# Performance work log

Measured on AMD Instinct MI355X. Metric: run time of the kernel, lower is better.

## Reference

```python
import jax, jax.numpy as jnp
import numpy as np

B, T, E, H = 4, 2048, 1024, 16
HD = E // H  # 64


def setup_inputs() -> dict:
    key = jax.random.key(0)
    ks = jax.random.split(key, 7)
    s = 0.02
    return {
        "values": jax.random.normal(ks[0], (B, T, E), jnp.float32),
        "keys": jax.random.normal(ks[1], (B, T, E), jnp.float32),
        "query": jax.random.normal(ks[2], (B, T, E), jnp.float32),
        "Wv": jax.random.normal(ks[3], (HD, HD), jnp.float32) * s,
        "Wk": jax.random.normal(ks[4], (HD, HD), jnp.float32) * s,
        "Wq": jax.random.normal(ks[5], (HD, HD), jnp.float32) * s,
        "Wo": jax.random.normal(ks[6], (E, E), jnp.float32) * s,
    }


def _proj_split(x, W):
    # x: [B,T,E] -> per-head projection with shared [HD,HD] weight -> [B,H,T,HD]
    xh = x.reshape(B, T, H, HD)
    return jnp.einsum("bthd,ed->bhte", xh, W)  # torch Linear: x @ W.T


def reference(values, keys, query, Wv, Wk, Wq, Wo):
    v = _proj_split(values, Wv)   # [B,H,T,HD]
    k = _proj_split(keys, Wk)
    q = _proj_split(query, Wq)
    scale = 1.0 / np.sqrt(HD).astype(np.float32)
    scores = jnp.einsum("bhqd,bhkd->bhqk", q, k) * scale  # [B,H,T,T]
    probs = jax.nn.softmax(scores, axis=-1)
    attn = jnp.einsum("bhqk,bhkd->bhqd", probs, v)        # [B,H,T,HD]
    out = attn.transpose(0, 2, 1, 3).reshape(B, T, E)      # combine heads
    return out @ Wo.T
```

## Files before the change

### kernel.cpp

```cpp
#include <hip/hip_runtime.h>


typedef __bf16 bf16x8 __attribute__((ext_vector_type(8)));
typedef float f32x4 __attribute__((ext_vector_type(4)));
typedef float f32x16 __attribute__((ext_vector_type(16)));
typedef unsigned int u32x2v __attribute__((ext_vector_type(2)));
typedef unsigned int u32x4v __attribute__((ext_vector_type(4)));

#define DEVI static __device__ __forceinline__

constexpr int Bc = 4, Tc = 2048, Ec = 1024, HDc = 64;
constexpr int BHc = 64;

DEVI unsigned short f2bf(float f) {
  unsigned int u = __builtin_bit_cast(unsigned int, f);
  u += 0x7fffu + ((u >> 16) & 1u);
  return (unsigned short)(u >> 16);
}

DEVI int swzf(int row) { return (row & 7) ^ ((row >> 3) & 3); }

DEVI bf16x8 lds_frag(const unsigned short* base, int row, int chunk) {
  const char* p = reinterpret_cast<const char*>(base) + row * 128 + ((chunk ^ swzf(row)) * 16);
  return *reinterpret_cast<const bf16x8*>(p);
}
DEVI void lds_store16(unsigned short* base, int row, int ci, uint4 v) {
  char* p = reinterpret_cast<char*>(base) + row * 128 + ((ci ^ swzf(row)) * 16);
  *reinterpret_cast<uint4*>(p) = v;
}
DEVI uint4 pack8(float4 a, float4 b) {
  uint4 o;
  o.x = f2bf(a.x) | ((unsigned)f2bf(a.y) << 16);
  o.y = f2bf(a.z) | ((unsigned)f2bf(a.w) << 16);
  o.z = f2bf(b.x) | ((unsigned)f2bf(b.y) << 16);
  o.w = f2bf(b.z) | ((unsigned)f2bf(b.w) << 16);
  return o;
}

DEVI unsigned cvt_pk_bf16(float lo, float hi) {
  unsigned r;
  asm("v_cvt_pk_bf16_f32 %0, %1, %2" : "=v"(r) : "v"(lo), "v"(hi));
  return r;
}
DEVI float exp2_fast(float x) {
  float r;
  asm("v_exp_f32 %0, %1" : "=v"(r) : "v"(x));
  return r;
}
DEVI void plswap(unsigned& a, unsigned& b) {
#if __has_builtin(__builtin_amdgcn_permlane32_swap)
  u32x2v r = __builtin_amdgcn_permlane32_swap(a, b, false, false);
  a = r.x; b = r.y;
#else
  int lane = threadIdx.x & 63;
  unsigned sa = (unsigned)__shfl_xor((int)a, 32), sb = (unsigned)__shfl_xor((int)b, 32);
  unsigned na = (lane < 32) ? a : sb;
  unsigned nb = (lane < 32) ? sa : b;
  a = na; b = nb;
#endif
}

DEVI void gload16(const unsigned short* g, unsigned short* l) {
  __builtin_amdgcn_global_load_lds(
      (const __attribute__((address_space(1))) void*)g,
      (__attribute__((address_space(3))) void*)l, 16, 0, 0);
}

__global__ __launch_bounds__(256) void proj3_kernel(
    const float* __restrict__ xv, const float* __restrict__ xk,
    const float* __restrict__ xq, const float* __restrict__ Wv,
    const float* __restrict__ Wk, const float* __restrict__ Wq,
    unsigned short* __restrict__ ov, unsigned short* __restrict__ ok,
    unsigned short* __restrict__ oq, float qscale) {
  const int which = blockIdx.z;
  const float* x = which == 0 ? xv : which == 1 ? xk : xq;
  const float* W = which == 0 ? Wv : which == 1 ? Wk : Wq;
  unsigned short* out = which == 0 ? ov : which == 1 ? ok : oq;
  const int transposed = (which == 0);
  const float wscale = (which == 2) ? qscale : 1.0f;

  __shared__ __align__(16) unsigned short Xl[64 * 64];
  __shared__ __align__(16) unsigned short Wl[64 * 64];
  const int tid = threadIdx.x;
  const int bh = blockIdx.y, t0 = blockIdx.x * 64;
  const int b = bh >> 4, h = bh & 15;
  const float* xbase = x + (size_t)(b * Tc + t0) * Ec + h * HDc;

#pragma unroll
  for (int it = 0; it < 2; ++it) {
    int ch = tid + it * 256;
    int row = ch >> 3, ci = ch & 7;
    float4 wa = *reinterpret_cast<const float4*>(W + row * 64 + ci * 8);
    float4 wb = *reinterpret_cast<const float4*>(W + row * 64 + ci * 8 + 4);
    wa.x *= wscale; wa.y *= wscale; wa.z *= wscale; wa.w *= wscale;
    wb.x *= wscale; wb.y *= wscale; wb.z *= wscale; wb.w *= wscale;
    lds_store16(Wl, row, ci, pack8(wa, wb));
    float4 xa = *reinterpret_cast<const float4*>(xbase + (size_t)row * Ec + ci * 8);
    float4 xb = *reinterpret_cast<const float4*>(xbase + (size_t)row * Ec + ci * 8 + 4);
    lds_store16(Xl, row, ci, pack8(xa, xb));
  }
  __syncthreads();

  const int lane = tid & 63, wv = tid >> 6;
  const int c16 = lane & 15, hi = lane >> 4;
  f32x4 acc[4];
#pragma unroll
  for (int nb = 0; nb < 4; ++nb) acc[nb] = {0.f, 0.f, 0.f, 0.f};
  if (!transposed) {
#pragma unroll
    for (int c = 0; c < 2; ++c) {
      bf16x8 aX = lds_frag(Xl, 16 * wv + c16, 4 * c + hi);
#pragma unroll
      for (int nb = 0; nb < 4; ++nb) {
        bf16x8 bW = lds_frag(Wl, 16 * nb + c16, 4 * c + hi);
        acc[nb] = __builtin_amdgcn_mfma_f32_16x16x32_bf16(aX, bW, acc[nb], 0, 0, 0);
      }
    }
#pragma unroll
    for (int nb = 0; nb < 4; ++nb)
#pragma unroll
      for (int r = 0; r < 4; ++r) {
        int t = t0 + 16 * wv + 4 * hi + r;
        int e = 16 * nb + c16;
        out[(size_t)(bh * Tc + t) * HDc + e] = f2bf(acc[nb][r]);
      }
  } else {
#pragma unroll
    for (int c = 0; c < 2; ++c) {
      bf16x8 aW = lds_frag(Wl, 16 * wv + c16, 4 * c + hi);
#pragma unroll
      for (int nb = 0; nb < 4; ++nb) {
        bf16x8 bX = lds_frag(Xl, 16 * nb + c16, 4 * c + hi);
        acc[nb] = __builtin_amdgcn_mfma_f32_16x16x32_bf16(aW, bX, acc[nb], 0, 0, 0);
      }
    }
#pragma unroll
    for (int nb = 0; nb < 4; ++nb)
#pragma unroll
      for (int r = 0; r < 4; ++r) {
        int e = 16 * wv + 4 * hi + r;
        int t = t0 + 16 * nb + c16;
        out[(size_t)(bh * HDc + e) * Tc + t] = f2bf(acc[nb][r]);
      }
  }
}

__global__ __launch_bounds__(256) void cast_wo(const float* __restrict__ Wsrc,
                                               unsigned short* __restrict__ dst) {
  size_t i = (size_t)blockIdx.x * 256 + threadIdx.x;
  float4 f = *reinterpret_cast<const float4*>(Wsrc + i * 4);
  uint2 o;
  o.x = f2bf(f.x) | ((unsigned)f2bf(f.y) << 16);
  o.y = f2bf(f.z) | ((unsigned)f2bf(f.w) << 16);
  *reinterpret_cast<uint2*>(dst + i * 4) = o;
}

DEVI void stage_kv(const unsigned short* __restrict__ Kp,
                   const unsigned short* __restrict__ Vp, int kt,
                   unsigned short* Kl, unsigned short* Vl, int wv, int lane) {
#pragma unroll
  for (int j = 0; j < 2; ++j) {
    const int base = (4 * j + wv) * 64;
    const int slot = base + lane;
    const int row = slot >> 3;
    const int sc = ((slot & 7) ^ swzf(row)) * 8;
    gload16(Kp + (size_t)(kt * 64 + row) * 64 + sc, Kl + base * 8);
    gload16(Vp + (size_t)row * Tc + kt * 64 + sc, Vl + base * 8);
  }
}

DEVI void exp_pf(f32x16& s0, f32x16& s1, bf16x8 pf[4]) {
#pragma unroll
  for (int i = 0; i < 16; ++i) s0[i] = exp2_fast(s0[i]);
#pragma unroll
  for (int i = 0; i < 16; ++i) s1[i] = exp2_fast(s1[i]);
  unsigned w0[8], w1[8];
#pragma unroll
  for (int i = 0; i < 8; ++i) w0[i] = cvt_pk_bf16(s0[2 * i], s0[2 * i + 1]);
#pragma unroll
  for (int i = 0; i < 8; ++i) w1[i] = cvt_pk_bf16(s1[2 * i], s1[2 * i + 1]);
  plswap(w0[0], w0[2]); plswap(w0[1], w0[3]); plswap(w0[4], w0[6]); plswap(w0[5], w0[7]);
  plswap(w1[0], w1[2]); plswap(w1[1], w1[3]); plswap(w1[4], w1[6]); plswap(w1[5], w1[7]);
  pf[0] = __builtin_bit_cast(bf16x8, (u32x4v){w0[0], w0[1], w0[2], w0[3]});
  pf[1] = __builtin_bit_cast(bf16x8, (u32x4v){w0[4], w0[5], w0[6], w0[7]});
  pf[2] = __builtin_bit_cast(bf16x8, (u32x4v){w1[0], w1[1], w1[2], w1[3]});
  pf[3] = __builtin_bit_cast(bf16x8, (u32x4v){w1[4], w1[5], w1[6], w1[7]});
}

__global__ __launch_bounds__(256, 2) void attn_kernel(
    const unsigned short* __restrict__ Qb_, const unsigned short* __restrict__ Kb_,
    const unsigned short* __restrict__ Vtb_, unsigned short* __restrict__ O) {
  __shared__ __align__(16) unsigned short KV[2][2][64 * 64];
  const int tid = threadIdx.x, lane = tid & 63, wv = tid >> 6;
  const int c32 = lane & 31, hi = lane >> 5;
  const int flat = blockIdx.y * (int)gridDim.x + blockIdx.x;
  const int logical = (flat & 7) * 64 + (flat >> 3);
  const int q0 = (logical & 7) * 256, bh = logical >> 3;
  const int b = bh >> 4, h = bh & 15;
  const unsigned short* Qp = Qb_ + (size_t)bh * Tc * HDc;
  const unsigned short* Kp = Kb_ + (size_t)bh * Tc * HDc;
  const unsigned short* Vp = Vtb_ + (size_t)bh * HDc * Tc;

  stage_kv(Kp, Vp, 0, KV[0][0], KV[0][1], wv, lane);

  const int tA = q0 + 64 * wv + c32, tB = tA + 32;
  bf16x8 qfA[4], qfB[4];
#pragma unroll
  for (int c = 0; c < 4; ++c) {
    qfA[c] = *reinterpret_cast<const bf16x8*>(Qp + (size_t)tA * HDc + 16 * c + 8 * hi);
    qfB[c] = *reinterpret_cast<const bf16x8*>(Qp + (size_t)tB * HDc + 16 * c + 8 * hi);
  }

  f32x16 aA0, aA1, aB0, aB1, lAacc, lBacc;
#pragma unroll
  for (int i = 0; i < 16; ++i) {
    aA0[i] = 0.f; aA1[i] = 0.f; aB0[i] = 0.f; aB1[i] = 0.f;
    lAacc[i] = 0.f; lBacc[i] = 0.f;
  }
  const u32x4v onesu = {0x3F803F80u, 0x3F803F80u, 0x3F803F80u, 0x3F803F80u};
  const bf16x8 ones = __builtin_bit_cast(bf16x8, onesu);

  auto tile = [&](const unsigned short* Kl, const unsigned short* Vl) {
    f32x16 sA0, sA1, sB0, sB1;
#pragma unroll
    for (int i = 0; i < 16; ++i) { sA0[i] = 0.f; sA1[i] = 0.f; sB0[i] = 0.f; sB1[i] = 0.f; }
    __builtin_amdgcn_s_setprio(1);
#pragma unroll
    for (int c = 0; c < 4; ++c) {
      bf16x8 k0 = lds_frag(Kl, c32, 2 * c + hi);
      sA0 = __builtin_amdgcn_mfma_f32_32x32x16_bf16(k0, qfA[c], sA0, 0, 0, 0);
      sB0 = __builtin_amdgcn_mfma_f32_32x32x16_bf16(k0, qfB[c], sB0, 0, 0, 0);
      bf16x8 k1 = lds_frag(Kl, 32 + c32, 2 * c + hi);
      sA1 = __builtin_amdgcn_mfma_f32_32x32x16_bf16(k1, qfA[c], sA1, 0, 0, 0);
      sB1 = __builtin_amdgcn_mfma_f32_32x32x16_bf16(k1, qfB[c], sB1, 0, 0, 0);
    }
    __builtin_amdgcn_s_setprio(0);
    bf16x8 pfA[4], pfB[4];
    exp_pf(sA0, sA1, pfA);
    exp_pf(sB0, sB1, pfB);
    __builtin_amdgcn_s_setprio(1);
#pragma unroll
    for (int ks = 0; ks < 4; ++ks) {
      bf16x8 v0 = lds_frag(Vl, c32, 2 * ks + hi);
      aA0 = __builtin_amdgcn_mfma_f32_32x32x16_bf16(v0, pfA[ks], aA0, 0, 0, 0);
      aB0 = __builtin_amdgcn_mfma_f32_32x32x16_bf16(v0, pfB[ks], aB0, 0, 0, 0);
      bf16x8 v1 = lds_frag(Vl, 32 + c32, 2 * ks + hi);
      aA1 = __builtin_amdgcn_mfma_f32_32x32x16_bf16(v1, pfA[ks], aA1, 0, 0, 0);
      aB1 = __builtin_amdgcn_mfma_f32_32x32x16_bf16(v1, pfB[ks], aB1, 0, 0, 0);
      lAacc = __builtin_amdgcn_mfma_f32_32x32x16_bf16(ones, pfA[ks], lAacc, 0, 0, 0);
      lBacc = __builtin_amdgcn_mfma_f32_32x32x16_bf16(ones, pfB[ks], lBacc, 0, 0, 0);
    }
    __builtin_amdgcn_s_setprio(0);
  };

  constexpr int NT = Tc / 64;
  __syncthreads();
  for (int kt = 0; kt < NT; kt += 2) {
    stage_kv(Kp, Vp, kt + 1, KV[1][0], KV[1][1], wv, lane);
    tile(KV[0][0], KV[0][1]);
    __syncthreads();
    if (kt + 2 < NT) stage_kv(Kp, Vp, kt + 2, KV[0][0], KV[0][1], wv, lane);
    tile(KV[1][0], KV[1][1]);
    __syncthreads();
  }

  {
    const float rl = 1.0f / lAacc[0];
    unsigned short* orow = O + (size_t)(b * Tc + tA) * Ec + h * HDc;
#pragma unroll
    for (int rq = 0; rq < 4; ++rq) {
      uint2 p0, p1;
      p0.x = cvt_pk_bf16(aA0[4 * rq] * rl, aA0[4 * rq + 1] * rl);
      p0.y = cvt_pk_bf16(aA0[4 * rq + 2] * rl, aA0[4 * rq + 3] * rl);
      *reinterpret_cast<uint2*>(orow + 8 * rq + 4 * hi) = p0;
      p1.x = cvt_pk_bf16(aA1[4 * rq] * rl, aA1[4 * rq + 1] * rl);
      p1.y = cvt_pk_bf16(aA1[4 * rq + 2] * rl, aA1[4 * rq + 3] * rl);
      *reinterpret_cast<uint2*>(orow + 32 + 8 * rq + 4 * hi) = p1;
    }
  }
  {
    const float rl = 1.0f / lBacc[0];
    unsigned short* orow = O + (size_t)(b * Tc + tB) * Ec + h * HDc;
#pragma unroll
    for (int rq = 0; rq < 4; ++rq) {
      uint2 p0, p1;
      p0.x = cvt_pk_bf16(aB0[4 * rq] * rl, aB0[4 * rq + 1] * rl);
      p0.y = cvt_pk_bf16(aB0[4 * rq + 2] * rl, aB0[4 * rq + 3] * rl);
      *reinterpret_cast<uint2*>(orow + 8 * rq + 4 * hi) = p0;
      p1.x = cvt_pk_bf16(aB1[4 * rq] * rl, aB1[4 * rq + 1] * rl);
      p1.y = cvt_pk_bf16(aB1[4 * rq + 2] * rl, aB1[4 * rq + 3] * rl);
      *reinterpret_cast<uint2*>(orow + 32 + 8 * rq + 4 * hi) = p1;
    }
  }
}

DEVI void stage_ab(const unsigned short* __restrict__ Ap,
                   const unsigned short* __restrict__ Bp, int kt,
                   unsigned short* Al, unsigned short* Bl, int wv, int lane) {
#pragma unroll
  for (int j = 0; j < 4; ++j) {
    const int base = (4 * j + wv) * 64;
    const int slot = base + lane;
    const int row = slot >> 3;
    const int sc = ((slot & 7) ^ swzf(row)) * 8;
    gload16(Ap + (size_t)row * Ec + kt * 64 + sc, Al + base * 8);
    gload16(Bp + (size_t)row * Ec + kt * 64 + sc, Bl + base * 8);
  }
}

__global__ __launch_bounds__(256, 2) void ogemm_kernel(
    const unsigned short* __restrict__ A, const unsigned short* __restrict__ Bw,
    float* __restrict__ out) {
  __shared__ __align__(16) unsigned short Al[2][128 * 64];
  __shared__ __align__(16) unsigned short Bl[2][128 * 64];
  const int tid = threadIdx.x, lane = tid & 63, wv = tid >> 6;
  const int c32 = lane & 31, hi = lane >> 5;
  const int flat = blockIdx.y * (int)gridDim.x + blockIdx.x;
  const int logical = (flat & 7) * 64 + (flat >> 3);
  const int n0 = (logical & 7) * 128, m0 = (logical >> 3) * 128;
  const int wr = wv >> 1, wc = wv & 1;
  const unsigned short* Ap = A + (size_t)m0 * Ec;
  const unsigned short* Bp = Bw + (size_t)n0 * Ec;

  f32x16 acc[2][2];
#pragma unroll
  for (int mi = 0; mi < 2; ++mi)
#pragma unroll
    for (int ni = 0; ni < 2; ++ni)
#pragma unroll
      for (int i = 0; i < 16; ++i) acc[mi][ni][i] = 0.f;

  auto gtile = [&](const unsigned short* Alc, const unsigned short* Blc) {
    __builtin_amdgcn_s_setprio(1);
#pragma unroll
    for (int kc = 0; kc < 4; ++kc) {
      bf16x8 x0 = lds_frag(Alc, 64 * wr + c32, 2 * kc + hi);
      bf16x8 x1 = lds_frag(Alc, 64 * wr + 32 + c32, 2 * kc + hi);
      bf16x8 y0 = lds_frag(Blc, 64 * wc + c32, 2 * kc + hi);
      bf16x8 y1 = lds_frag(Blc, 64 * wc + 32 + c32, 2 * kc + hi);
      acc[0][0] = __builtin_amdgcn_mfma_f32_32x32x16_bf16(x0, y0, acc[0][0], 0, 0, 0);
      acc[0][1] = __builtin_amdgcn_mfma_f32_32x32x16_bf16(x0, y1, acc[0][1], 0, 0, 0);
      acc[1][0] = __builtin_amdgcn_mfma_f32_32x32x16_bf16(x1, y0, acc[1][0], 0, 0, 0);
      acc[1][1] = __builtin_amdgcn_mfma_f32_32x32x16_bf16(x1, y1, acc[1][1], 0, 0, 0);
    }
    __builtin_amdgcn_s_setprio(0);
  };

  stage_ab(Ap, Bp, 0, Al[0], Bl[0], wv, lane);
  __syncthreads();
  for (int kt = 0; kt < Ec / 64; kt += 2) {
    stage_ab(Ap, Bp, kt + 1, Al[1], Bl[1], wv, lane);
    gtile(Al[0], Bl[0]);
    __syncthreads();
    if (kt + 2 < Ec / 64) stage_ab(Ap, Bp, kt + 2, Al[0], Bl[0], wv, lane);
    gtile(Al[1], Bl[1]);
    __syncthreads();
  }

  const int nb = n0 + 64 * wc + c32;
  const int mb = m0 + 64 * wr + 4 * hi;
#pragma unroll
  for (int mi = 0; mi < 2; ++mi)
#pragma unroll
    for (int ni = 0; ni < 2; ++ni)
#pragma unroll
      for (int rq = 0; rq < 4; ++rq)
#pragma unroll
        for (int j = 0; j < 4; ++j) {
          int mrow = mb + 32 * mi + 8 * rq + j;
          out[(size_t)mrow * Ec + nb + 32 * ni] = acc[mi][ni][4 * rq + j];
        }
}

extern "C" void kernel_launch(void* const* d_in, const int* in_sizes, int n_in,
                              void* d_out, int out_size, void* d_ws, size_t ws_size,
                              hipStream_t stream) {
  (void)in_sizes; (void)n_in; (void)out_size; (void)ws_size;
  const float* values = (const float*)d_in[0];
  const float* keys   = (const float*)d_in[1];
  const float* query  = (const float*)d_in[2];
  const float* Wv = (const float*)d_in[3];
  const float* Wk = (const float*)d_in[4];
  const float* Wq = (const float*)d_in[5];
  const float* Wo = (const float*)d_in[6];
  float* out = (float*)d_out;

  char* ws = (char*)d_ws;
  constexpr size_t SZ = (size_t)BHc * Tc * HDc * 2;
  unsigned short* qb  = (unsigned short*)(ws + 0 * SZ);
  unsigned short* kb  = (unsigned short*)(ws + 1 * SZ);
  unsigned short* vt  = (unsigned short*)(ws + 2 * SZ);
  unsigned short* at  = (unsigned short*)(ws + 3 * SZ);
  unsigned short* wob = (unsigned short*)(ws + 4 * SZ);

  dim3 blk(256);
  proj3_kernel<<<dim3(Tc / 64, BHc, 3), blk, 0, stream>>>(
      values, keys, query, Wv, Wk, Wq, vt, kb, qb, 0.18033688011112042f);
  cast_wo<<<dim3(Ec * Ec / 1024), blk, 0, stream>>>(Wo, wob);
  attn_kernel<<<dim3(Tc / 256, BHc), blk, 0, stream>>>(qb, kb, vt, at);
  ogemm_kernel<<<dim3(Ec / 128, (Bc * Tc) / 128), blk, 0, stream>>>(at, wob, out);
}
```

Before: 129.0 us.

## Replace ones-MFMA row sums with VALU sums and deepen KV pipeline

The softmax denominator is now accumulated with VALU adds over the exponentiated scores plus a cross-half permlane swap at the end, instead of two extra MFMAs per k-step against a vector of ones. The first QK MFMA takes a shared zero accumulator, which removes the per-tile zeroing. KV staging moves to four LDS buffers processed in pairs, so each pair of tiles needs one barrier instead of two and loads run further ahead. The cost is twice the LDS footprint, which may reduce occupancy, and extra VALU work for the row sums, whose accumulation order differs from the MFMA sum.

```diff
diff --git a/kernel.cpp b/kernel.cpp
--- a/kernel.cpp
+++ b/kernel.cpp
@@ -58,6 +58,11 @@
   unsigned nb = (lane < 32) ? sa : b;
   a = na; b = nb;
 #endif
+}
+DEVI float halfsum(float x) {
+  unsigned a = __builtin_bit_cast(unsigned, x), b = a;
+  plswap(a, b);
+  return __builtin_bit_cast(float, a) + __builtin_bit_cast(float, b);
 }
 
 DEVI void gload16(const unsigned short* g, unsigned short* l) {
@@ -169,11 +174,19 @@
   }
 }
 
-DEVI void exp_pf(f32x16& s0, f32x16& s1, bf16x8 pf[4]) {
+DEVI float exp_sum_pf(f32x16& s0, f32x16& s1, bf16x8 pf[4]) {
 #pragma unroll
   for (int i = 0; i < 16; ++i) s0[i] = exp2_fast(s0[i]);
 #pragma unroll
   for (int i = 0; i < 16; ++i) s1[i] = exp2_fast(s1[i]);
+  float t[16];
+#pragma unroll
+  for (int i = 0; i < 16; ++i) t[i] = s0[i] + s1[i];
+#pragma unroll
+  for (int i = 0; i < 8; ++i) t[i] += t[i + 8];
+#pragma unroll
+  for (int i = 0; i < 4; ++i) t[i] += t[i + 4];
+  float rs = (t[0] + t[1]) + (t[2] + t[3]);
   unsigned w0[8], w1[8];
 #pragma unroll
   for (int i = 0; i < 8; ++i) w0[i] = cvt_pk_bf16(s0[2 * i], s0[2 * i + 1]);
@@ -185,12 +198,13 @@
   pf[1] = __builtin_bit_cast(bf16x8, (u32x4v){w0[4], w0[5], w0[6], w0[7]});
   pf[2] = __builtin_bit_cast(bf16x8, (u32x4v){w1[0], w1[1], w1[2], w1[3]});
   pf[3] = __builtin_bit_cast(bf16x8, (u32x4v){w1[4], w1[5], w1[6], w1[7]});
+  return rs;
 }
 
 __global__ __launch_bounds__(256, 2) void attn_kernel(
     const unsigned short* __restrict__ Qb_, const unsigned short* __restrict__ Kb_,
     const unsigned short* __restrict__ Vtb_, unsigned short* __restrict__ O) {
-  __shared__ __align__(16) unsigned short KV[2][2][64 * 64];
+  __shared__ __align__(16) unsigned short KV[4][2][64 * 64];
   const int tid = threadIdx.x, lane = tid & 63, wv = tid >> 6;
   const int c32 = lane & 31, hi = lane >> 5;
   const int flat = blockIdx.y * (int)gridDim.x + blockIdx.x;
@@ -202,6 +216,7 @@
   const unsigned short* Vp = Vtb_ + (size_t)bh * HDc * Tc;
 
   stage_kv(Kp, Vp, 0, KV[0][0], KV[0][1], wv, lane);
+  stage_kv(Kp, Vp, 1, KV[1][0], KV[1][1], wv, lane);
 
   const int tA = q0 + 64 * wv + c32, tB = tA + 32;
   bf16x8 qfA[4], qfB[4];
@@ -211,22 +226,26 @@
     qfB[c] = *reinterpret_cast<const bf16x8*>(Qp + (size_t)tB * HDc + 16 * c + 8 * hi);
   }
 
-  f32x16 aA0, aA1, aB0, aB1, lAacc, lBacc;
+  f32x16 aA0, aA1, aB0, aB1, zv;
 #pragma unroll
   for (int i = 0; i < 16; ++i) {
-    aA0[i] = 0.f; aA1[i] = 0.f; aB0[i] = 0.f; aB1[i] = 0.f;
-    lAacc[i] = 0.f; lBacc[i] = 0.f;
-  }
-  const u32x4v onesu = {0x3F803F80u, 0x3F803F80u, 0x3F803F80u, 0x3F803F80u};
-  const bf16x8 ones = __builtin_bit_cast(bf16x8, onesu);
+    aA0[i] = 0.f; aA1[i] = 0.f; aB0[i] = 0.f; aB1[i] = 0.f; zv[i] = 0.f;
+  }
+  float lA = 0.f, lB = 0.f;
 
   auto tile = [&](const unsigned short* Kl, const unsigned short* Vl) {
     f32x16 sA0, sA1, sB0, sB1;
-#pragma unroll
-    for (int i = 0; i < 16; ++i) { sA0[i] = 0.f; sA1[i] = 0.f; sB0[i] = 0.f; sB1[i] = 0.f; }
     __builtin_amdgcn_s_setprio(1);
-#pragma unroll
-    for (int c = 0; c < 4; ++c) {
+    {
+      bf16x8 k0 = lds_frag(Kl, c32, hi);
+      sA0 = __builtin_amdgcn_mfma_f32_32x32x16_bf16(k0, qfA[0], zv, 0, 0, 0);
+      sB0 = __builtin_amdgcn_mfma_f32_32x32x16_bf16(k0, qfB[0], zv, 0, 0, 0);
+      bf16x8 k1 = lds_frag(Kl, 32 + c32, hi);
+      sA1 = __builtin_amdgcn_mfma_f32_32x32x16_bf16(k1, qfA[0], zv, 0, 0, 0);
+      sB1 = __builtin_amdgcn_mfma_f32_32x32x16_bf16(k1, qfB[0], zv, 0, 0, 0);
+    }
+#pragma unroll
+    for (int c = 1; c < 4; ++c) {
       bf16x8 k0 = lds_frag(Kl, c32, 2 * c + hi);
       sA0 = __builtin_amdgcn_mfma_f32_32x32x16_bf16(k0, qfA[c], sA0, 0, 0, 0);
       sB0 = __builtin_amdgcn_mfma_f32_32x32x16_bf16(k0, qfB[c], sB0, 0, 0, 0);
@@ -236,8 +255,8 @@
     }
     __builtin_amdgcn_s_setprio(0);
     bf16x8 pfA[4], pfB[4];
-    exp_pf(sA0, sA1, pfA);
-    exp_pf(sB0, sB1, pfB);
+    lA += exp_sum_pf(sA0, sA1, pfA);
+    lB += exp_sum_pf(sB0, sB1, pfB);
     __builtin_amdgcn_s_setprio(1);
 #pragma unroll
     for (int ks = 0; ks < 4; ++ks) {
@@ -247,25 +266,26 @@
       bf16x8 v1 = lds_frag(Vl, 32 + c32, 2 * ks + hi);
       aA1 = __builtin_amdgcn_mfma_f32_32x32x16_bf16(v1, pfA[ks], aA1, 0, 0, 0);
       aB1 = __builtin_amdgcn_mfma_f32_32x32x16_bf16(v1, pfB[ks], aB1, 0, 0, 0);
-      lAacc = __builtin_amdgcn_mfma_f32_32x32x16_bf16(ones, pfA[ks], lAacc, 0, 0, 0);
-      lBacc = __builtin_amdgcn_mfma_f32_32x32x16_bf16(ones, pfB[ks], lBacc, 0, 0, 0);
     }
     __builtin_amdgcn_s_setprio(0);
   };
 
-  constexpr int NT = Tc / 64;
+  constexpr int NP = Tc / 128;
   __syncthreads();
-  for (int kt = 0; kt < NT; kt += 2) {
-    stage_kv(Kp, Vp, kt + 1, KV[1][0], KV[1][1], wv, lane);
-    tile(KV[0][0], KV[0][1]);
+  for (int kp = 0; kp < NP; ++kp) {
+    const int cb = (kp & 1) << 1;
+    const int sb = cb ^ 2;
+    if (kp + 1 < NP) {
+      stage_kv(Kp, Vp, 2 * kp + 2, KV[sb][0], KV[sb][1], wv, lane);
+      stage_kv(Kp, Vp, 2 * kp + 3, KV[sb + 1][0], KV[sb + 1][1], wv, lane);
+    }
+    tile(KV[cb][0], KV[cb][1]);
+    tile(KV[cb + 1][0], KV[cb + 1][1]);
     __syncthreads();
-    if (kt + 2 < NT) stage_kv(Kp, Vp, kt + 2, KV[0][0], KV[0][1], wv, lane);
-    tile(KV[1][0], KV[1][1]);
-    __syncthreads();
   }
 
   {
-    const float rl = 1.0f / lAacc[0];
+    const float rl = 1.0f / halfsum(lA);
     unsigned short* orow = O + (size_t)(b * Tc + tA) * Ec + h * HDc;
 #pragma unroll
     for (int rq = 0; rq < 4; ++rq) {
@@ -279,7 +299,7 @@
     }
   }
   {
-    const float rl = 1.0f / lBacc[0];
+    const float rl = 1.0f / halfsum(lB);
     unsigned short* orow = O + (size_t)(b * Tc + tB) * Ec + h * HDc;
 #pragma unroll
     for (int rq = 0; rq < 4; ++rq) {
```

New measurement: 147.8 us. 1.15x slower.
